# Performance work log

Measured on AMD Instinct MI355X. Metric: run time of the kernel, lower is better.

The kernel has to match this reference:

```python
import jax, jax.numpy as jnp
import numpy as np

N_NODES = 50000
N_EDGES = 800000
IN_CH = 128
MEAN_SIZE = 128
VAR_SIZE = 128


def setup_inputs() -> dict:
    key = jax.random.key(0)
    k_x, k_e, k_wm, k_wv = jax.random.split(key, 4)
    x = jax.random.normal(k_x, (N_NODES, IN_CH), dtype=jnp.float32)
    edge_index = jax.random.randint(k_e, (2, N_EDGES), 0, N_NODES, dtype=jnp.int32)
    # torch Linear(2*C, M, bias=False) weight has shape [M, 2*C]
    s = 1.0 / np.sqrt(2 * IN_CH)
    w_mean = jax.random.uniform(k_wm, (MEAN_SIZE, 2 * IN_CH), jnp.float32, -s, s)
    w_var = jax.random.uniform(k_wv, (VAR_SIZE, 2 * IN_CH), jnp.float32, -s, s)
    return {"x": x, "edge_index": edge_index, "w_mean": w_mean, "w_var": w_var}


def reference(x, edge_index, w_mean, w_var):
    row, col = edge_index[0], edge_index[1]
    x_row = x[row]  # [E, C]
    x_col = x[col]  # [E, C]
    # cat([x_row, x_col], 1) @ W.T  ==  x_row @ W[:, :C].T + x_col @ W[:, C:].T
    C = x.shape[1]
    maps_mean = jnp.einsum('ec,mc->em', x_row, w_mean[:, :C]) + \
                jnp.einsum('ec,mc->em', x_col, w_mean[:, C:])
    maps_var = jnp.einsum('ec,vc->ev', x_row, w_var[:, :C]) + \
               jnp.einsum('ec,vc->ev', x_col, w_var[:, C:])
    return (maps_mean, maps_var)
```

## Files before the change

### kernel.cpp

```cpp
#include <hip/hip_runtime.h>
#include <hip/hip_bf16.h>

#define NODES 50000
#define EDGES 800000
#define CH 128
#define NCOL 512
#define MPAD 50048
#define EPW 4

typedef __attribute__((ext_vector_type(8))) __bf16 bf16x8;
typedef __attribute__((ext_vector_type(4))) float f32x4;
typedef unsigned long long u64;

static __device__ __forceinline__ unsigned short f2bf(float f) {
    union { float f; unsigned u; } v; v.f = f;
    unsigned r = v.u + 0x7FFFu + ((v.u >> 16) & 1u);
    return (unsigned short)(r >> 16);
}
static __device__ __forceinline__ float bf2f(unsigned short h) {
    union { unsigned u; float f; } v; v.u = ((unsigned)h) << 16;
    return v.f;
}

__global__ void k_cvt_x(const float* __restrict__ x, unsigned short* __restrict__ xb) {
    int i = blockIdx.x * blockDim.x + threadIdx.x;
    if (i >= MPAD * CH / 4) return;
    int base = i << 2;
    unsigned short s0 = 0, s1 = 0, s2 = 0, s3 = 0;
    if (base < NODES * CH) {
        const f32x4 v = *reinterpret_cast<const f32x4*>(x + base);
        s0 = f2bf(v[0]); s1 = f2bf(v[1]); s2 = f2bf(v[2]); s3 = f2bf(v[3]);
    }
    u64 p = (u64)s0 | ((u64)s1 << 16) | ((u64)s2 << 32) | ((u64)s3 << 48);
    *reinterpret_cast<u64*>(xb + base) = p;
}

__global__ void k_pack_w(const float* __restrict__ wm, const float* __restrict__ wv,
                         unsigned short* __restrict__ wb) {
    int i = blockIdx.x * blockDim.x + threadIdx.x;
    if (i >= NCOL * CH) return;
    int n = i >> 7, k = i & 127;
    float v;
    if (n < 128)      v = wm[n * 256 + k];
    else if (n < 256) v = wm[(n - 128) * 256 + 128 + k];
    else if (n < 384) v = wv[(n - 256) * 256 + k];
    else              v = wv[(n - 384) * 256 + 128 + k];
    wb[i] = f2bf(v);
}

__global__ __launch_bounds__(256) void k_gemm(const unsigned short* __restrict__ xb,
                                              const unsigned short* __restrict__ wb,
                                              unsigned short* __restrict__ th) {
    const int lane = threadIdx.x & 63;
    const int wave = threadIdx.x >> 6;
    const int rowbase = blockIdx.x * 128 + (wave >> 1) * 64;
    const int colbase = blockIdx.y * 128 + (wave & 1) * 64;
    const int lr = lane & 15;
    const int kg = lane >> 4;
    f32x4 acc[4][4] = {};
#pragma unroll
    for (int ks = 0; ks < 4; ++ks) {
        const int k = ks * 32 + kg * 8;
        bf16x8 af[4], bfr[4];
#pragma unroll
        for (int a = 0; a < 4; ++a)
            af[a] = *reinterpret_cast<const bf16x8*>(xb + (size_t)(rowbase + a * 16 + lr) * CH + k);
#pragma unroll
        for (int b = 0; b < 4; ++b)
            bfr[b] = *reinterpret_cast<const bf16x8*>(wb + (size_t)(colbase + b * 16 + lr) * CH + k);
#pragma unroll
        for (int a = 0; a < 4; ++a)
#pragma unroll
            for (int b = 0; b < 4; ++b)
                acc[a][b] = __builtin_amdgcn_mfma_f32_16x16x32_bf16(af[a], bfr[b], acc[a][b], 0, 0, 0);
    }
    const int crow = (lane >> 4) * 4;
    const int ccol = lane & 15;
#pragma unroll
    for (int a = 0; a < 4; ++a)
#pragma unroll
        for (int b = 0; b < 4; ++b)
#pragma unroll
            for (int j = 0; j < 4; ++j) {
                int row = rowbase + a * 16 + crow + j;
                int col = colbase + b * 16 + ccol;
                th[(size_t)row * NCOL + col] = f2bf(acc[a][b][j]);
            }
}

template <int HALF>
__global__ __launch_bounds__(256) void k_edges_p(const int* __restrict__ ei,
                                                 const unsigned short* __restrict__ th,
                                                 float* __restrict__ out) {
    const int wave = threadIdx.x >> 6;
    const int lane = threadIdx.x & 63;
    const int es = lane >> 5;
    const int j = lane & 31;
    const int ebase = (blockIdx.x * 4 + wave) * (2 * EPW);

    int rr[EPW], cc[EPW];
#pragma unroll
    for (int i = 0; i < EPW; ++i) {
        int e = ebase + 2 * i + es;
        rr[i] = ei[e];
        cc[i] = ei[EDGES + e];
    }
    u64 pa[EPW], pb[EPW];
#pragma unroll
    for (int i = 0; i < EPW; ++i) {
        pa[i] = *reinterpret_cast<const u64*>(th + (size_t)rr[i] * NCOL + HALF * 256 + j * 4);
        pb[i] = *reinterpret_cast<const u64*>(th + (size_t)cc[i] * NCOL + HALF * 256 + 128 + j * 4);
    }
    const size_t obase = (size_t)HALF * ((size_t)EDGES * 128) + (size_t)j * 4;
#pragma unroll
    for (int i = 0; i < EPW; ++i) {
        const int e = ebase + 2 * i + es;
        f32x4 s;
        s[0] = bf2f((unsigned short)pa[i])         + bf2f((unsigned short)pb[i]);
        s[1] = bf2f((unsigned short)(pa[i] >> 16)) + bf2f((unsigned short)(pb[i] >> 16));
        s[2] = bf2f((unsigned short)(pa[i] >> 32)) + bf2f((unsigned short)(pb[i] >> 32));
        s[3] = bf2f((unsigned short)(pa[i] >> 48)) + bf2f((unsigned short)(pb[i] >> 48));
        __builtin_nontemporal_store(
            s, reinterpret_cast<f32x4*>(out + obase + (size_t)e * 128));
    }
}

__global__ void k_naive(const float* __restrict__ x, const int* __restrict__ ei,
                        const float* __restrict__ wm, const float* __restrict__ wv,
                        float* __restrict__ out) {
    __shared__ float xs[256];
    int e = blockIdx.x;
    int t = threadIdx.x;
    int r = ei[e], c = ei[EDGES + e];
    xs[t] = (t < 128) ? x[(size_t)r * 128 + t] : x[(size_t)c * 128 + (t - 128)];
    __syncthreads();
    const float* w = (t < 128) ? (wm + (size_t)t * 256) : (wv + (size_t)(t - 128) * 256);
    float acc = 0.f;
#pragma unroll 8
    for (int k = 0; k < 256; ++k) acc = fmaf(xs[k], w[k], acc);
    size_t ooff = (t < 128) ? ((size_t)e * 128 + t)
                            : ((size_t)EDGES * 128 + (size_t)e * 128 + (t - 128));
    out[ooff] = acc;
}

extern "C" void kernel_launch(void* const* d_in, const int* in_sizes, int n_in,
                              void* d_out, int out_size, void* d_ws, size_t ws_size,
                              hipStream_t stream) {
    const float* x  = (const float*)d_in[0];
    const int*   ei = (const int*)d_in[1];
    const float* wm = (const float*)d_in[2];
    const float* wv = (const float*)d_in[3];
    float* out = (float*)d_out;

    const size_t xb_b = (size_t)MPAD * CH * 2;
    const size_t wb_b = (size_t)NCOL * CH * 2;
    const size_t th_b = (size_t)MPAD * NCOL * 2;

    if (ws_size < xb_b + wb_b + th_b) {
        k_naive<<<EDGES, 256, 0, stream>>>(x, ei, wm, wv, out);
        return;
    }

    unsigned short* xb  = (unsigned short*)d_ws;
    unsigned short* wb  = (unsigned short*)((char*)d_ws + xb_b);
    unsigned short* tab = (unsigned short*)((char*)d_ws + xb_b + wb_b);

    k_cvt_x<<<(MPAD * CH / 4 + 255) / 256, 256, 0, stream>>>(x, xb);
    k_pack_w<<<(NCOL * CH + 255) / 256, 256, 0, stream>>>(wm, wv, wb);
    dim3 g(MPAD / 128, NCOL / 128);
    k_gemm<<<g, 256, 0, stream>>>(xb, wb, tab);

    const int eb = EDGES / (4 * 2 * EPW);
    k_edges_p<0><<<eb, 256, 0, stream>>>(ei, tab, out);
    k_edges_p<1><<<eb, 256, 0, stream>>>(ei, tab, out);
}
```

Measured before the change: 267.2 us.

## Quantize per-node projection table to int8 with per-row scales and merge edge passes

The per-node projection table moves from bf16 to int8 with one scale per row and half. Each GEMM block now covers all 512 output columns for 64 rows, computes per-row absmax through shuffles and shared memory, then writes the quantized rows out coalesced. The two per-half edge kernels become one kernel that gathers int8 rows, dequantizes them and writes both outputs, which halves gather bytes and drops a launch. In exchange it adds int8 quantization error on top of bf16, which may break accuracy tolerance.

```diff
diff --git a/kernel.cpp b/kernel.cpp
--- a/kernel.cpp
+++ b/kernel.cpp
@@ -6,20 +6,18 @@
 #define CH 128
 #define NCOL 512
 #define MPAD 50048
+#define QROWS 64
 #define EPW 4
 
 typedef __attribute__((ext_vector_type(8))) __bf16 bf16x8;
 typedef __attribute__((ext_vector_type(4))) float f32x4;
+typedef __attribute__((ext_vector_type(2))) float f32x2;
 typedef unsigned long long u64;
 
 static __device__ __forceinline__ unsigned short f2bf(float f) {
     union { float f; unsigned u; } v; v.f = f;
     unsigned r = v.u + 0x7FFFu + ((v.u >> 16) & 1u);
     return (unsigned short)(r >> 16);
-}
-static __device__ __forceinline__ float bf2f(unsigned short h) {
-    union { unsigned u; float f; } v; v.u = ((unsigned)h) << 16;
-    return v.f;
 }
 
 __global__ void k_cvt_x(const float* __restrict__ x, unsigned short* __restrict__ xb) {
@@ -48,49 +46,99 @@
     wb[i] = f2bf(v);
 }
 
-__global__ __launch_bounds__(256) void k_gemm(const unsigned short* __restrict__ xb,
-                                              const unsigned short* __restrict__ wb,
-                                              unsigned short* __restrict__ th) {
+__global__ __launch_bounds__(256) void k_gemmq(const unsigned short* __restrict__ xb,
+                                               const unsigned short* __restrict__ wb,
+                                               char* __restrict__ qt,
+                                               float* __restrict__ sc) {
+    __shared__ float sM[2][2][QROWS];
+    __shared__ __align__(16) char sQ[QROWS][NCOL];
     const int lane = threadIdx.x & 63;
     const int wave = threadIdx.x >> 6;
-    const int rowbase = blockIdx.x * 128 + (wave >> 1) * 64;
-    const int colbase = blockIdx.y * 128 + (wave & 1) * 64;
+    const int rowbase = blockIdx.x * QROWS;
     const int lr = lane & 15;
     const int kg = lane >> 4;
-    f32x4 acc[4][4] = {};
+
+    f32x4 acc[4][8] = {};
 #pragma unroll
     for (int ks = 0; ks < 4; ++ks) {
         const int k = ks * 32 + kg * 8;
-        bf16x8 af[4], bfr[4];
+        bf16x8 af[4], bfr[8];
 #pragma unroll
         for (int a = 0; a < 4; ++a)
             af[a] = *reinterpret_cast<const bf16x8*>(xb + (size_t)(rowbase + a * 16 + lr) * CH + k);
 #pragma unroll
-        for (int b = 0; b < 4; ++b)
-            bfr[b] = *reinterpret_cast<const bf16x8*>(wb + (size_t)(colbase + b * 16 + lr) * CH + k);
-#pragma unroll
-        for (int a = 0; a < 4; ++a)
-#pragma unroll
-            for (int b = 0; b < 4; ++b)
+        for (int b = 0; b < 8; ++b)
+            bfr[b] = *reinterpret_cast<const bf16x8*>(wb + (size_t)(wave * 128 + lr * 8 + b) * CH + k);
+#pragma unroll
+        for (int a = 0; a < 4; ++a)
+#pragma unroll
+            for (int b = 0; b < 8; ++b)
                 acc[a][b] = __builtin_amdgcn_mfma_f32_16x16x32_bf16(af[a], bfr[b], acc[a][b], 0, 0, 0);
     }
+
     const int crow = (lane >> 4) * 4;
     const int ccol = lane & 15;
+    const int half = wave >> 1;
+
+    float m[4][4];
 #pragma unroll
     for (int a = 0; a < 4; ++a)
 #pragma unroll
-        for (int b = 0; b < 4; ++b)
-#pragma unroll
-            for (int j = 0; j < 4; ++j) {
-                int row = rowbase + a * 16 + crow + j;
-                int col = colbase + b * 16 + ccol;
-                th[(size_t)row * NCOL + col] = f2bf(acc[a][b][j]);
+        for (int j = 0; j < 4; ++j) {
+            float mm = 0.f;
+#pragma unroll
+            for (int b = 0; b < 8; ++b) mm = fmaxf(mm, fabsf(acc[a][b][j]));
+            m[a][j] = mm;
+        }
+#pragma unroll
+    for (int off = 1; off < 16; off <<= 1)
+#pragma unroll
+        for (int a = 0; a < 4; ++a)
+#pragma unroll
+            for (int j = 0; j < 4; ++j)
+                m[a][j] = fmaxf(m[a][j], __shfl_xor(m[a][j], off, 16));
+    if (ccol == 0)
+#pragma unroll
+        for (int a = 0; a < 4; ++a)
+#pragma unroll
+            for (int j = 0; j < 4; ++j)
+                sM[half][wave & 1][a * 16 + crow + j] = m[a][j];
+    __syncthreads();
+
+#pragma unroll
+    for (int a = 0; a < 4; ++a)
+#pragma unroll
+        for (int j = 0; j < 4; ++j) {
+            const int row = a * 16 + crow + j;
+            const float rm = fmaxf(sM[half][0][row], sM[half][1][row]);
+            const float inv = (rm > 1e-20f) ? 127.0f / rm : 0.0f;
+            u64 pk = 0;
+#pragma unroll
+            for (int b = 0; b < 8; ++b) {
+                int q = __float2int_rn(acc[a][b][j] * inv);
+                q = max(-127, min(127, q));
+                pk |= (u64)((unsigned)q & 0xFFu) << (8 * b);
             }
-}
-
-template <int HALF>
-__global__ __launch_bounds__(256) void k_edges_p(const int* __restrict__ ei,
-                                                 const unsigned short* __restrict__ th,
+            *reinterpret_cast<u64*>(&sQ[row][wave * 128 + ccol * 8]) = pk;
+        }
+    if (threadIdx.x < 2 * QROWS) {
+        const int h = threadIdx.x >> 6, row = threadIdx.x & 63;
+        const float rm = fmaxf(sM[h][0][row], sM[h][1][row]);
+        sc[(size_t)(rowbase + row) * 2 + h] = (rm > 1e-20f) ? rm * (1.0f / 127.0f) : 1.0f;
+    }
+    __syncthreads();
+
+#pragma unroll
+    for (int t = 0; t < 8; ++t) {
+        const int off = t * 4096 + threadIdx.x * 16;
+        f32x4 v = *reinterpret_cast<const f32x4*>(&sQ[0][0] + off);
+        *reinterpret_cast<f32x4*>(qt + (size_t)rowbase * NCOL + off) = v;
+    }
+}
+
+__global__ __launch_bounds__(256) void k_edges_m(const int* __restrict__ ei,
+                                                 const char* __restrict__ qt,
+                                                 const float* __restrict__ sc,
                                                  float* __restrict__ out) {
     const int wave = threadIdx.x >> 6;
     const int lane = threadIdx.x & 63;
@@ -105,23 +153,35 @@
         rr[i] = ei[e];
         cc[i] = ei[EDGES + e];
     }
-    u64 pa[EPW], pb[EPW];
+    int am[EPW], av[EPW], bm[EPW], bv[EPW];
+    f32x2 sr[EPW], scl[EPW];
 #pragma unroll
     for (int i = 0; i < EPW; ++i) {
-        pa[i] = *reinterpret_cast<const u64*>(th + (size_t)rr[i] * NCOL + HALF * 256 + j * 4);
-        pb[i] = *reinterpret_cast<const u64*>(th + (size_t)cc[i] * NCOL + HALF * 256 + 128 + j * 4);
-    }
-    const size_t obase = (size_t)HALF * ((size_t)EDGES * 128) + (size_t)j * 4;
+        const char* qr = qt + (size_t)rr[i] * NCOL;
+        const char* qc = qt + (size_t)cc[i] * NCOL;
+        am[i] = *reinterpret_cast<const int*>(qr + j * 4);
+        av[i] = *reinterpret_cast<const int*>(qr + 256 + j * 4);
+        bm[i] = *reinterpret_cast<const int*>(qc + 128 + j * 4);
+        bv[i] = *reinterpret_cast<const int*>(qc + 384 + j * 4);
+        sr[i]  = *reinterpret_cast<const f32x2*>(sc + (size_t)rr[i] * 2);
+        scl[i] = *reinterpret_cast<const f32x2*>(sc + (size_t)cc[i] * 2);
+    }
 #pragma unroll
     for (int i = 0; i < EPW; ++i) {
         const int e = ebase + 2 * i + es;
-        f32x4 s;
-        s[0] = bf2f((unsigned short)pa[i])         + bf2f((unsigned short)pb[i]);
-        s[1] = bf2f((unsigned short)(pa[i] >> 16)) + bf2f((unsigned short)(pb[i] >> 16));
-        s[2] = bf2f((unsigned short)(pa[i] >> 32)) + bf2f((unsigned short)(pb[i] >> 32));
-        s[3] = bf2f((unsigned short)(pa[i] >> 48)) + bf2f((unsigned short)(pb[i] >> 48));
-        __builtin_nontemporal_store(
-            s, reinterpret_cast<f32x4*>(out + obase + (size_t)e * 128));
+        f32x4 sm_, sv_;
+#pragma unroll
+        for (int k = 0; k < 4; ++k) {
+            const int sh = 24 - 8 * k;
+            sm_[k] = sr[i][0] * (float)((am[i] << sh) >> 24)
+                   + scl[i][0] * (float)((bm[i] << sh) >> 24);
+            sv_[k] = sr[i][1] * (float)((av[i] << sh) >> 24)
+                   + scl[i][1] * (float)((bv[i] << sh) >> 24);
+        }
+        __builtin_nontemporal_store(sm_,
+            reinterpret_cast<f32x4*>(out + (size_t)e * 128 + j * 4));
+        __builtin_nontemporal_store(sv_,
+            reinterpret_cast<f32x4*>(out + (size_t)EDGES * 128 + (size_t)e * 128 + j * 4));
     }
 }
 
@@ -154,23 +214,21 @@
 
     const size_t xb_b = (size_t)MPAD * CH * 2;
     const size_t wb_b = (size_t)NCOL * CH * 2;
-    const size_t th_b = (size_t)MPAD * NCOL * 2;
-
-    if (ws_size < xb_b + wb_b + th_b) {
+    const size_t qt_b = (size_t)MPAD * NCOL;
+    const size_t sc_b = (size_t)MPAD * 2 * 4;
+
+    if (ws_size < xb_b + wb_b + qt_b + sc_b) {
         k_naive<<<EDGES, 256, 0, stream>>>(x, ei, wm, wv, out);
         return;
     }
 
-    unsigned short* xb  = (unsigned short*)d_ws;
-    unsigned short* wb  = (unsigned short*)((char*)d_ws + xb_b);
-    unsigned short* tab = (unsigned short*)((char*)d_ws + xb_b + wb_b);
+    unsigned short* xb = (unsigned short*)d_ws;
+    unsigned short* wb = (unsigned short*)((char*)d_ws + xb_b);
+    char*           qt = (char*)d_ws + xb_b + wb_b;
+    float*          sc = (float*)((char*)d_ws + xb_b + wb_b + qt_b);
 
     k_cvt_x<<<(MPAD * CH / 4 + 255) / 256, 256, 0, stream>>>(x, xb);
     k_pack_w<<<(NCOL * CH + 255) / 256, 256, 0, stream>>>(wm, wv, wb);
-    dim3 g(MPAD / 128, NCOL / 128);
-    k_gemm<<<g, 256, 0, stream>>>(xb, wb, tab);
-
-    const int eb = EDGES / (4 * 2 * EPW);
-    k_edges_p<0><<<eb, 256, 0, stream>>>(ei, tab, out);
-    k_edges_p<1><<<eb, 256, 0, stream>>>(ei, tab, out);
-}
+    k_gemmq<<<MPAD / QROWS, 256, 0, stream>>>(xb, wb, qt, sc);
+    k_edges_m<<<EDGES / (4 * 2 * EPW), 256, 0, stream>>>(ei, qt, sc, out);
+}
```

After: 226.5 us. 15.2% less time.
